# Kernel tuning notes

Hardware: AMD Instinct MI355X
Metric: run time of the kernel (lower is better)

## Reference

```python
import jax, jax.numpy as jnp
import numpy as np

B, C, COUT, L, K = 16, 64, 64, 16384, 3
STRIDE, PAD, DIL, G, DG = 1, 1, 1, 1, 1
LOUT = (L + 2 * PAD - DIL * (K - 1) - 1) // STRIDE + 1


def _conv1d(x, w, b, pad, groups):
    # x: [B, Cin, L], w: [Cout, Cin/groups, k] (torch Conv1d layout)
    y = jax.lax.conv_general_dilated(
        x, w, window_strides=(1,), padding=[(pad, pad)],
        dimension_numbers=('NCH', 'OIH', 'NCH'), feature_group_count=groups)
    return y + b[None, :, None]


def setup_inputs() -> dict:
    key = jax.random.key(0)
    k = jax.random.split(key, 11)
    s = jnp.float32(0.02)  # module init: normal(0, 0.02)
    return {
        'x': jax.random.normal(k[0], (B, C, L), jnp.float32),
        'w_off_dw': jax.random.normal(k[1], (C, 1, 7), jnp.float32) * s,
        'b_off_dw': jax.random.normal(k[2], (C,), jnp.float32) * s,
        'w_off_pw': jax.random.normal(k[3], (G * DG * K, C, 1), jnp.float32) * s,
        'b_off_pw': jax.random.normal(k[4], (G * DG * K,), jnp.float32) * s,
        'w_msk_dw': jax.random.normal(k[5], (C, 1, 7), jnp.float32) * s,
        'b_msk_dw': jax.random.normal(k[6], (C,), jnp.float32) * s,
        'w_msk_pw': jax.random.normal(k[7], (G * DG * K, C, 1), jnp.float32) * s,
        'b_msk_pw': jax.random.normal(k[8], (G * DG * K,), jnp.float32) * s,
        'weight': jax.random.normal(k[9], (COUT, C // G, K), jnp.float32) * s,
        'bias': jax.random.normal(k[10], (COUT,), jnp.float32) * s,
    }


def _deform_conv1d(x, w_off_dw, b_off_dw, w_off_pw, b_off_pw,
                   w_msk_dw, b_msk_dw, w_msk_pw, b_msk_pw, weight, bias):
    # offset / modulation-mask branches: depthwise k=7 conv -> 1x1 conv
    offset = _conv1d(_conv1d(x, w_off_dw, b_off_dw, 3, C), w_off_pw, b_off_pw, 0, 1)  # [B, G*DG*K, Lout]
    mask = jax.nn.sigmoid(_conv1d(_conv1d(x, w_msk_dw, b_msk_dw, 3, C), w_msk_pw, b_msk_pw, 0, 1))

    cpd = C // (G * DG)  # channels per deformable group
    off = jnp.repeat(offset.reshape(B, G * DG, K, LOUT), cpd, axis=1)  # [B, C, K, Lout]
    msk = jnp.repeat(mask.reshape(B, G * DG, K, LOUT), cpd, axis=1)

    base = jnp.arange(LOUT, dtype=x.dtype) * STRIDE - PAD  # [Lout]
    kpos = jnp.arange(K, dtype=x.dtype) * DIL              # [K]
    p = base[None, :] + kpos[:, None]                       # [K, Lout]
    p = p[None, None] + off                                 # fractional sample positions [B, C, K, Lout]

    i0 = jnp.floor(p)
    frac = p - i0
    i0i = i0.astype(jnp.int32)
    i1i = i0i + 1

    xb = jnp.broadcast_to(x[:, :, None, :], (B, C, K, L))
    x0 = jnp.take_along_axis(xb, jnp.clip(i0i, 0, L - 1), axis=-1)
    x1 = jnp.take_along_axis(xb, jnp.clip(i1i, 0, L - 1), axis=-1)
    v0 = ((i0i >= 0) & (i0i < L)).astype(x.dtype)  # zero padding outside
    v1 = ((i1i >= 0) & (i1i < L)).astype(x.dtype)

    # linear interpolation + mask modulation
    val = ((1.0 - frac) * x0 * v0 + frac * x1 * v1) * msk  # [B, C, K, Lout]

    # grouped contraction over (in-channels-per-group, kernel taps)
    out = jnp.einsum('bgikl,goik->bgol',
                     val.reshape(B, G, C // G, K, LOUT),
                     weight.reshape(G, COUT // G, C // G, K))
    return out.reshape(B, COUT, LOUT) + bias[None, :, None]


def reference(x, w_off_dw, b_off_dw, w_off_pw, b_off_pw,
              w_msk_dw, b_msk_dw, w_msk_pw, b_msk_pw, weight, bias):
    return _deform_conv1d(x, w_off_dw, b_off_dw, w_off_pw, b_off_pw,
                          w_msk_dw, b_msk_dw, w_msk_pw, b_msk_pw, weight, bias)
```

## Files before the change

### kernel.cpp

```cpp
#include <hip/hip_runtime.h>
#include <cstdint>

#define LX 16384
#define NB 16
#define LT 64
#define TPB 4
#define HALO 8
#define XI (LT + 2*HALO)
#define XPD 36

typedef __attribute__((ext_vector_type(2))) _Float16 h2;
typedef __attribute__((ext_vector_type(8))) _Float16 h8;
typedef __attribute__((ext_vector_type(4))) unsigned u4;
typedef __attribute__((ext_vector_type(4))) float f4;

static __device__ __forceinline__ h2 u2h(unsigned u) {
    union { unsigned u; h2 h; } v; v.u = u; return v.h;
}
static __device__ __forceinline__ unsigned h2u(h2 h) {
    union { h2 h; unsigned u; } v; v.h = h; return v.u;
}
static __device__ __forceinline__ unsigned pkrtz(float a, float b) {
    auto r = __builtin_amdgcn_cvt_pkrtz(a, b);
    union { decltype(r) h; unsigned u; } v; v.h = r;
    return v.u;
}

#define BAR_LGKM() do { asm volatile("s_waitcnt lgkmcnt(0)" ::: "memory"); \
                        __builtin_amdgcn_s_barrier();                      \
                        asm volatile("" ::: "memory"); } while (0)
#define BAR_RAW()  do { asm volatile("" ::: "memory");                     \
                        __builtin_amdgcn_s_barrier();                      \
                        asm volatile("" ::: "memory"); } while (0)

__global__ void prep_kernel(const float* __restrict__ weight,
                            const float* __restrict__ b_off_pw, const float* __restrict__ w_off_pw,
                            const float* __restrict__ b_off_dw,
                            const float* __restrict__ b_msk_pw, const float* __restrict__ w_msk_pw,
                            const float* __restrict__ b_msk_dw,
                            const float* __restrict__ w_off_dw, const float* __restrict__ w_msk_dw,
                            short* __restrict__ A2, float* __restrict__ beff,
                            unsigned* __restrict__ dwt2, unsigned* __restrict__ pwt2) {
    int bid = blockIdx.x;
    int t = threadIdx.x;
    if (bid < 48) {
        int idx = bid * 256 + t;
        int o = idx / 192;
        int rem = idx - o * 192;
        int tap = rem >> 6, c = rem & 63;
        union { _Float16 h; short s; } v;
        v.h = (_Float16)weight[o * 192 + c * 3 + tap];
        A2[idx] = v.s;
    } else {
        for (int idx = t; idx < 448; idx += 256) {
            int br = idx / 224, r2 = idx - br * 224;
            int j = r2 >> 5, cp = r2 & 31;
            const float* src = br ? w_msk_dw : w_off_dw;
            h2 h; h[0] = (_Float16)src[(2 * cp) * 7 + j]; h[1] = (_Float16)src[(2 * cp + 1) * 7 + j];
            dwt2[idx] = h2u(h);
        }
        if (t < 192) {
            int br = t / 96, r2 = t - br * 96;
            int m = r2 >> 5, cp = r2 & 31;
            const float* src = br ? w_msk_pw : w_off_pw;
            h2 h; h[0] = (_Float16)src[m * 64 + 2 * cp]; h[1] = (_Float16)src[m * 64 + 2 * cp + 1];
            pwt2[t] = h2u(h);
        }
        if (t < 6) {
            int br = t / 3, m = t % 3;
            const float* pw = br ? w_msk_pw : w_off_pw;
            const float* bd = br ? b_msk_dw : b_off_dw;
            const float* bp = br ? b_msk_pw : b_off_pw;
            float s = bp[m];
            for (int c = 0; c < 64; ++c) s += pw[m * 64 + c] * bd[c];
            beff[t] = s;
        }
    }
}

__launch_bounds__(256, 4)
__global__ void deform_main(const float* __restrict__ x,
                            const float* __restrict__ bias,
                            const short* __restrict__ A2,
                            const float* __restrict__ beff,
                            const unsigned* __restrict__ dwt2_g,
                            const unsigned* __restrict__ pwt2_g,
                            float* __restrict__ out) {
    __shared__ __align__(16) unsigned xdw[XI * XPD];
    __shared__ __align__(16) unsigned A2l[6144];
    __shared__ __align__(16) unsigned dwt2[448];
    __shared__ __align__(16) unsigned pwt2[192];
    __shared__ unsigned kl_wp[3][64];
    __shared__ int      kl_li[3][64];
    __shared__ float bias_l[64];
    __shared__ float beff_l[8];

    const int t = threadIdx.x;
    const int lbase = blockIdx.x * (LT * TPB);
    const int b = blockIdx.y;
    const float* xb = x + (size_t)b * (64 * LX);

    f4 rx0[3], rx1[3];

    auto issue_x = [&](int l0v) {
        #pragma unroll
        for (int s = 0; s < 3; ++s) {
            int p = t + 256 * s;
            rx0[s] = (f4){0.f, 0.f, 0.f, 0.f};
            rx1[s] = (f4){0.f, 0.f, 0.f, 0.f};
            if (p < 640) {
                int cp = p & 31, up = p >> 5;
                int g4 = l0v - HALO + up * 4;
                if ((unsigned)g4 < (unsigned)LX) {
                    rx0[s] = *(const f4*)(xb + (size_t)(2 * cp) * LX + g4);
                    rx1[s] = *(const f4*)(xb + (size_t)(2 * cp + 1) * LX + g4);
                }
            }
        }
    };
    auto write_x = [&]() {
        #pragma unroll
        for (int s = 0; s < 3; ++s) {
            int p = t + 256 * s;
            if (p < 640) {
                int cp = p & 31, up = p >> 5;
                #pragma unroll
                for (int d = 0; d < 4; ++d) {
                    int i = up * 4 + d;
                    int pc = ((cp >> 3) + i) & 3;
                    xdw[i * XPD + pc * 8 + (cp & 7)] = pkrtz(rx0[s][d], rx1[s][d]);
                }
            }
        }
    };

    issue_x(lbase);
    {
        const u4* A2g4 = (const u4*)A2;
        #pragma unroll
        for (int s = 0; s < 6; ++s) {
            int idx = t + 256 * s;
            int row = idx / 24;
            int g = idx - row * 24;
            int pdw = row * 96 + ((g * 4) ^ ((row & 7) << 2));
            *(u4*)&A2l[pdw] = A2g4[idx];
        }
    }
    for (int idx = t; idx < 448; idx += 256) dwt2[idx] = dwt2_g[idx];
    if (t < 192) pwt2[t] = pwt2_g[t];
    if (t < 64) bias_l[t] = bias[t];
    if (t < 6)  beff_l[t] = beff[t];
    write_x();
    issue_x(lbase + LT);
    BAR_LGKM();

    #pragma unroll
    for (int tt = 0; tt < TPB; ++tt) {
        const int l0 = lbase + tt * LT;

        {
            const int l = t >> 2, cc = t & 3;
            h2 so2[8], sm2[8];
            #pragma unroll
            for (int m = 0; m < 8; ++m) { so2[m] = (h2)(_Float16)0; sm2[m] = (h2)(_Float16)0; }
            #pragma unroll
            for (int j = 0; j < 7; ++j) {
                int i = l + 5 + j;
                const unsigned* xr = &xdw[i * XPD + (((cc + i) & 3) << 3)];
                u4 xa = *(const u4*)xr;
                u4 xb2 = *(const u4*)(xr + 4);
                const unsigned* wo = &dwt2[j * 32 + cc * 8];
                const unsigned* wm = &dwt2[224 + j * 32 + cc * 8];
                u4 woa = *(const u4*)wo, wob = *(const u4*)(wo + 4);
                u4 wma = *(const u4*)wm, wmb = *(const u4*)(wm + 4);
                #pragma unroll
                for (int m = 0; m < 4; ++m) {
                    so2[m]     += u2h(xa[m])  * u2h(woa[m]);
                    so2[m + 4] += u2h(xb2[m]) * u2h(wob[m]);
                    sm2[m]     += u2h(xa[m])  * u2h(wma[m]);
                    sm2[m + 4] += u2h(xb2[m]) * u2h(wmb[m]);
                }
            }
            float po[3] = {0.f, 0.f, 0.f}, pm[3] = {0.f, 0.f, 0.f};
            #pragma unroll
            for (int m3 = 0; m3 < 3; ++m3) {
                const unsigned* p0 = &pwt2[m3 * 32 + cc * 8];
                const unsigned* p1 = &pwt2[96 + m3 * 32 + cc * 8];
                u4 a0 = *(const u4*)p0, a1 = *(const u4*)(p0 + 4);
                u4 b0 = *(const u4*)p1, b1 = *(const u4*)(p1 + 4);
                #pragma unroll
                for (int m = 0; m < 4; ++m) {
                    po[m3] = __builtin_amdgcn_fdot2(so2[m],     u2h(a0[m]), po[m3], false);
                    po[m3] = __builtin_amdgcn_fdot2(so2[m + 4], u2h(a1[m]), po[m3], false);
                    pm[m3] = __builtin_amdgcn_fdot2(sm2[m],     u2h(b0[m]), pm[m3], false);
                    pm[m3] = __builtin_amdgcn_fdot2(sm2[m + 4], u2h(b1[m]), pm[m3], false);
                }
            }
            #pragma unroll
            for (int d = 1; d <= 2; d <<= 1) {
                #pragma unroll
                for (int m3 = 0; m3 < 3; ++m3) {
                    po[m3] += __shfl_xor(po[m3], d);
                    pm[m3] += __shfl_xor(pm[m3], d);
                }
            }
            if (cc < 3) {
                int k = cc;
                float off = (k == 0 ? po[0] : k == 1 ? po[1] : po[2]) + beff_l[k];
                float z   = (k == 0 ? pm[0] : k == 1 ? pm[1] : pm[2]) + beff_l[3 + k];
                float msk = 1.0f / (1.0f + __expf(-z));
                float p = (float)(l0 + l - 1 + k) + off;
                float fl = floorf(p);
                int i0 = (int)fl, i1 = i0 + 1;
                float fr = p - fl;
                int li0 = i0 - l0 + HALO, li1 = li0 + 1;
                float w0 = (((unsigned)i0 < (unsigned)LX) && ((unsigned)li0 < (unsigned)XI)) ? (1.0f - fr) * msk : 0.0f;
                float w1 = (((unsigned)i1 < (unsigned)LX) && ((unsigned)li1 < (unsigned)XI)) ? fr * msk : 0.0f;
                li0 = min(max(li0, 0), XI - 2);
                kl_wp[k][l] = pkrtz(w0, w1);
                kl_li[k][l] = li0;
            }
        }
        BAR_LGKM();

        {
            const int lane = t & 63;
            const int wv = t >> 6;
            const int r = lane & 15, q = lane >> 4;
            const int lcol = wv * 16 + r;

            h8 bfr[6];
            #pragma unroll
            for (int kk = 0; kk < 6; ++kk) {
                const int tap = kk >> 1;
                unsigned wp = kl_wp[tap][lcol];
                unsigned w00 = __builtin_amdgcn_perm(wp, wp, 0x01000100u);
                unsigned w11 = __builtin_amdgcn_perm(wp, wp, 0x03020302u);
                int li0 = kl_li[tap][lcol];
                int cp0 = (((kk & 1) << 5) + (q << 3)) >> 1;
                int chunkL = cp0 >> 3;
                int o0 = li0 * XPD + ((((chunkL + li0) & 3) << 3) | (cp0 & 7));
                int o1 = (li0 + 1) * XPD + ((((chunkL + li0 + 1) & 3) << 3) | (cp0 & 7));
                u4 r0 = *(const u4*)&xdw[o0];
                u4 r1 = *(const u4*)&xdw[o1];
                u4 xs;
                #pragma unroll
                for (int d = 0; d < 4; ++d)
                    xs[d] = h2u(u2h(r0[d]) * u2h(w00) + u2h(r1[d]) * u2h(w11));
                union { u4 u; h8 h; } cvt; cvt.u = xs;
                bfr[kk] = cvt.h;
            }

            #pragma unroll
            for (int mt = 0; mt < 4; ++mt) {
                f4 acc = {0.f, 0.f, 0.f, 0.f};
                const int row = mt * 16 + r;
                const int rowbase = row * 96;
                const int sw = (r & 7) << 2;
                #pragma unroll
                for (int kk = 0; kk < 6; ++kk) {
                    union { u4 u; h8 h; } af;
                    af.u = *(const u4*)&A2l[rowbase + ((kk * 16 + q * 4) ^ sw)];
                    acc = __builtin_amdgcn_mfma_f32_16x16x32_f16(af.h, bfr[kk], acc, 0, 0, 0);
                }
                int ob = mt * 16 + 4 * q;
                float* op = out + ((size_t)b * 64 + ob) * LX + l0 + lcol;
                #pragma unroll
                for (int e = 0; e < 4; ++e)
                    op[(size_t)e * LX] = acc[e] + bias_l[ob + e];
            }
        }

        if (tt < TPB - 1) {
            BAR_RAW();
            write_x();
            if (tt + 2 < TPB) issue_x(lbase + (tt + 2) * LT);
            BAR_LGKM();
        }
    }
}

extern "C" void kernel_launch(void* const* d_in, const int* in_sizes, int n_in,
                              void* d_out, int out_size, void* d_ws, size_t ws_size,
                              hipStream_t stream) {
    const float* x        = (const float*)d_in[0];
    const float* w_off_dw = (const float*)d_in[1];
    const float* b_off_dw = (const float*)d_in[2];
    const float* w_off_pw = (const float*)d_in[3];
    const float* b_off_pw = (const float*)d_in[4];
    const float* w_msk_dw = (const float*)d_in[5];
    const float* b_msk_dw = (const float*)d_in[6];
    const float* w_msk_pw = (const float*)d_in[7];
    const float* b_msk_pw = (const float*)d_in[8];
    const float* weight   = (const float*)d_in[9];
    const float* bias     = (const float*)d_in[10];
    float* out = (float*)d_out;

    short*    A2   = (short*)d_ws;
    float*    beff = (float*)((char*)d_ws + 24576);
    unsigned* dwt2 = (unsigned*)((char*)d_ws + 24608);
    unsigned* pwt2 = (unsigned*)((char*)d_ws + 26400);

    hipLaunchKernelGGL(prep_kernel, dim3(49), dim3(256), 0, stream,
                       weight, b_off_pw, w_off_pw, b_off_dw, b_msk_pw, w_msk_pw, b_msk_dw,
                       w_off_dw, w_msk_dw, A2, beff, dwt2, pwt2);
    hipLaunchKernelGGL(deform_main, dim3(LX / (LT * TPB), NB), dim3(256), 0, stream,
                       x, bias, A2, beff, dwt2, pwt2, out);
}
```

Before: 154.4 us.

## Fold depthwise+pointwise offset/mask convs into one MFMA and drop LDS staging

Precomputes combined depthwise×pointwise weights so the offset and mask branches become a single 16x16x32 MFMA chain over 7 taps and 64 channels, held as register fragments, replacing the packed-half FMA and fdot2 path. The per-position sample weights and indices are passed between lanes with shuffles instead of through shared memory, which removes a barrier per tile. The main contraction loop is reordered so each interpolated B fragment feeds four accumulators directly. This raises register pressure (14 u4 weight fragments plus 4 accumulators) under the 4-waves launch bound, and the folded weights are rounded to fp16 as products rather than separately.

Measured after the change: 191.2 us. +23.8%, slower.

```diff
diff --git a/kernel.cpp b/kernel.cpp
--- a/kernel.cpp
+++ b/kernel.cpp
@@ -40,7 +40,7 @@
                             const float* __restrict__ b_msk_dw,
                             const float* __restrict__ w_off_dw, const float* __restrict__ w_msk_dw,
                             short* __restrict__ A2, float* __restrict__ beff,
-                            unsigned* __restrict__ dwt2, unsigned* __restrict__ pwt2) {
+                            unsigned* __restrict__ wcg) {
     int bid = blockIdx.x;
     int t = threadIdx.x;
     if (bid < 48) {
@@ -52,27 +52,29 @@
         v.h = (_Float16)weight[o * 192 + c * 3 + tap];
         A2[idx] = v.s;
     } else {
-        for (int idx = t; idx < 448; idx += 256) {
-            int br = idx / 224, r2 = idx - br * 224;
-            int j = r2 >> 5, cp = r2 & 31;
-            const float* src = br ? w_msk_dw : w_off_dw;
-            h2 h; h[0] = (_Float16)src[(2 * cp) * 7 + j]; h[1] = (_Float16)src[(2 * cp + 1) * 7 + j];
-            dwt2[idx] = h2u(h);
-        }
-        if (t < 192) {
-            int br = t / 96, r2 = t - br * 96;
-            int m = r2 >> 5, cp = r2 & 31;
-            const float* src = br ? w_msk_pw : w_off_pw;
-            h2 h; h[0] = (_Float16)src[m * 64 + 2 * cp]; h[1] = (_Float16)src[m * 64 + 2 * cp + 1];
-            pwt2[t] = h2u(h);
+        int lane = t >> 2, d = t & 3;
+        int m = lane & 15, qq = lane >> 4;
+        #pragma unroll
+        for (int s = 0; s < 14; ++s) {
+            int j = s >> 1;
+            int c = (s & 1) * 32 + qq * 8 + 2 * d;
+            float w0 = 0.f, w1 = 0.f;
+            if (m < 3) {
+                w0 = w_off_pw[m * 64 + c]     * w_off_dw[c * 7 + j];
+                w1 = w_off_pw[m * 64 + c + 1] * w_off_dw[(c + 1) * 7 + j];
+            } else if (m < 6) {
+                w0 = w_msk_pw[(m - 3) * 64 + c]     * w_msk_dw[c * 7 + j];
+                w1 = w_msk_pw[(m - 3) * 64 + c + 1] * w_msk_dw[(c + 1) * 7 + j];
+            }
+            wcg[s * 256 + t] = pkrtz(w0, w1);
         }
         if (t < 6) {
-            int br = t / 3, m = t % 3;
+            int br = t / 3, m3 = t % 3;
             const float* pw = br ? w_msk_pw : w_off_pw;
             const float* bd = br ? b_msk_dw : b_off_dw;
             const float* bp = br ? b_msk_pw : b_off_pw;
-            float s = bp[m];
-            for (int c = 0; c < 64; ++c) s += pw[m * 64 + c] * bd[c];
+            float s = bp[m3];
+            for (int c = 0; c < 64; ++c) s += pw[m3 * 64 + c] * bd[c];
             beff[t] = s;
         }
     }
@@ -83,19 +85,17 @@
                             const float* __restrict__ bias,
                             const short* __restrict__ A2,
                             const float* __restrict__ beff,
-                            const unsigned* __restrict__ dwt2_g,
-                            const unsigned* __restrict__ pwt2_g,
+                            const unsigned* __restrict__ wcg,
                             float* __restrict__ out) {
     __shared__ __align__(16) unsigned xdw[XI * XPD];
     __shared__ __align__(16) unsigned A2l[6144];
-    __shared__ __align__(16) unsigned dwt2[448];
-    __shared__ __align__(16) unsigned pwt2[192];
-    __shared__ unsigned kl_wp[3][64];
-    __shared__ int      kl_li[3][64];
     __shared__ float bias_l[64];
     __shared__ float beff_l[8];
 
     const int t = threadIdx.x;
+    const int lane = t & 63;
+    const int wv = t >> 6;
+    const int r = lane & 15, q = lane >> 4;
     const int lbase = blockIdx.x * (LT * TPB);
     const int b = blockIdx.y;
     const float* xb = x + (size_t)b * (64 * LX);
@@ -146,8 +146,12 @@
             *(u4*)&A2l[pdw] = A2g4[idx];
         }
     }
-    for (int idx = t; idx < 448; idx += 256) dwt2[idx] = dwt2_g[idx];
-    if (t < 192) pwt2[t] = pwt2_g[t];
+    u4 wfr[14];
+    {
+        const u4* wc4 = (const u4*)wcg;
+        #pragma unroll
+        for (int s = 0; s < 14; ++s) wfr[s] = wc4[s * 64 + lane];
+    }
     if (t < 64) bias_l[t] = bias[t];
     if (t < 6)  beff_l[t] = beff[t];
     write_x();
@@ -158,56 +162,30 @@
     for (int tt = 0; tt < TPB; ++tt) {
         const int l0 = lbase + tt * LT;
 
+        unsigned mywp = 0; int myli = 0;
         {
-            const int l = t >> 2, cc = t & 3;
-            h2 so2[8], sm2[8];
-            #pragma unroll
-            for (int m = 0; m < 8; ++m) { so2[m] = (h2)(_Float16)0; sm2[m] = (h2)(_Float16)0; }
-            #pragma unroll
-            for (int j = 0; j < 7; ++j) {
-                int i = l + 5 + j;
-                const unsigned* xr = &xdw[i * XPD + (((cc + i) & 3) << 3)];
-                u4 xa = *(const u4*)xr;
-                u4 xb2 = *(const u4*)(xr + 4);
-                const unsigned* wo = &dwt2[j * 32 + cc * 8];
-                const unsigned* wm = &dwt2[224 + j * 32 + cc * 8];
-                u4 woa = *(const u4*)wo, wob = *(const u4*)(wo + 4);
-                u4 wma = *(const u4*)wm, wmb = *(const u4*)(wm + 4);
-                #pragma unroll
-                for (int m = 0; m < 4; ++m) {
-                    so2[m]     += u2h(xa[m])  * u2h(woa[m]);
-                    so2[m + 4] += u2h(xb2[m]) * u2h(wob[m]);
-                    sm2[m]     += u2h(xa[m])  * u2h(wma[m]);
-                    sm2[m + 4] += u2h(xb2[m]) * u2h(wmb[m]);
-                }
-            }
-            float po[3] = {0.f, 0.f, 0.f}, pm[3] = {0.f, 0.f, 0.f};
-            #pragma unroll
-            for (int m3 = 0; m3 < 3; ++m3) {
-                const unsigned* p0 = &pwt2[m3 * 32 + cc * 8];
-                const unsigned* p1 = &pwt2[96 + m3 * 32 + cc * 8];
-                u4 a0 = *(const u4*)p0, a1 = *(const u4*)(p0 + 4);
-                u4 b0 = *(const u4*)p1, b1 = *(const u4*)(p1 + 4);
-                #pragma unroll
-                for (int m = 0; m < 4; ++m) {
-                    po[m3] = __builtin_amdgcn_fdot2(so2[m],     u2h(a0[m]), po[m3], false);
-                    po[m3] = __builtin_amdgcn_fdot2(so2[m + 4], u2h(a1[m]), po[m3], false);
-                    pm[m3] = __builtin_amdgcn_fdot2(sm2[m],     u2h(b0[m]), pm[m3], false);
-                    pm[m3] = __builtin_amdgcn_fdot2(sm2[m + 4], u2h(b1[m]), pm[m3], false);
-                }
-            }
-            #pragma unroll
-            for (int d = 1; d <= 2; d <<= 1) {
-                #pragma unroll
-                for (int m3 = 0; m3 < 3; ++m3) {
-                    po[m3] += __shfl_xor(po[m3], d);
-                    pm[m3] += __shfl_xor(pm[m3], d);
-                }
-            }
-            if (cc < 3) {
-                int k = cc;
-                float off = (k == 0 ? po[0] : k == 1 ? po[1] : po[2]) + beff_l[k];
-                float z   = (k == 0 ? pm[0] : k == 1 ? pm[1] : pm[2]) + beff_l[3 + k];
+            f4 acc2 = {0.f, 0.f, 0.f, 0.f};
+            const int irow = wv * 16 + r + 5;
+            #pragma unroll
+            for (int s = 0; s < 14; ++s) {
+                const int j = s >> 1, half = s & 1;
+                const int i = irow + j;
+                const int chunk = half * 2 + (q >> 1);
+                const int pd = i * XPD + (((chunk + i) & 3) << 3) + ((q & 1) << 2);
+                union { u4 u; h8 h; } bx; bx.u = *(const u4*)&xdw[pd];
+                union { u4 u; h8 h; } ax; ax.u = wfr[s];
+                acc2 = __builtin_amdgcn_mfma_f32_16x16x32_f16(ax.h, bx.h, acc2, 0, 0, 0);
+            }
+            float b0 = __shfl(acc2[0], r);
+            float b1 = __shfl(acc2[1], r);
+            float b2 = __shfl(acc2[2], r);
+            float m0 = __shfl(acc2[3], r);
+            float m1 = __shfl(acc2[0], 16 + r);
+            float m2 = __shfl(acc2[1], 16 + r);
+            if (q < 3) {
+                const int k = q, l = wv * 16 + r;
+                float off = (k == 0 ? b0 : k == 1 ? b1 : b2) + beff_l[k];
+                float z   = (k == 0 ? m0 : k == 1 ? m1 : m2) + beff_l[3 + k];
                 float msk = 1.0f / (1.0f + __expf(-z));
                 float p = (float)(l0 + l - 1 + k) + off;
                 float fl = floorf(p);
@@ -217,27 +195,31 @@
                 float w0 = (((unsigned)i0 < (unsigned)LX) && ((unsigned)li0 < (unsigned)XI)) ? (1.0f - fr) * msk : 0.0f;
                 float w1 = (((unsigned)i1 < (unsigned)LX) && ((unsigned)li1 < (unsigned)XI)) ? fr * msk : 0.0f;
                 li0 = min(max(li0, 0), XI - 2);
-                kl_wp[k][l] = pkrtz(w0, w1);
-                kl_li[k][l] = li0;
-            }
-        }
-        BAR_LGKM();
+                mywp = pkrtz(w0, w1);
+                myli = li0;
+            }
+        }
 
         {
-            const int lane = t & 63;
-            const int wv = t >> 6;
-            const int r = lane & 15, q = lane >> 4;
             const int lcol = wv * 16 + r;
-
-            h8 bfr[6];
+            unsigned wpt[3]; int lit[3];
+            #pragma unroll
+            for (int tap = 0; tap < 3; ++tap) {
+                wpt[tap] = __shfl(mywp, tap * 16 + r);
+                lit[tap] = __shfl(myli, tap * 16 + r);
+            }
+            f4 acc[4];
+            #pragma unroll
+            for (int mt = 0; mt < 4; ++mt) acc[mt] = (f4){0.f, 0.f, 0.f, 0.f};
+            const int sw = (r & 7) << 2;
             #pragma unroll
             for (int kk = 0; kk < 6; ++kk) {
                 const int tap = kk >> 1;
-                unsigned wp = kl_wp[tap][lcol];
+                unsigned wp = wpt[tap];
                 unsigned w00 = __builtin_amdgcn_perm(wp, wp, 0x01000100u);
                 unsigned w11 = __builtin_amdgcn_perm(wp, wp, 0x03020302u);
-                int li0 = kl_li[tap][lcol];
-                int cp0 = (((kk & 1) << 5) + (q << 3)) >> 1;
+                int li0 = lit[tap];
+                int cp0 = ((kk & 1) << 4) + (q << 2);
                 int chunkL = cp0 >> 3;
                 int o0 = li0 * XPD + ((((chunkL + li0) & 3) << 3) | (cp0 & 7));
                 int o1 = (li0 + 1) * XPD + ((((chunkL + li0 + 1) & 3) << 3) | (cp0 & 7));
@@ -247,27 +229,21 @@
                 #pragma unroll
                 for (int d = 0; d < 4; ++d)
                     xs[d] = h2u(u2h(r0[d]) * u2h(w00) + u2h(r1[d]) * u2h(w11));
-                union { u4 u; h8 h; } cvt; cvt.u = xs;
-                bfr[kk] = cvt.h;
-            }
-
+                union { u4 u; h8 h; } bfr; bfr.u = xs;
+                #pragma unroll
+                for (int mt = 0; mt < 4; ++mt) {
+                    union { u4 u; h8 h; } af;
+                    af.u = *(const u4*)&A2l[(mt * 16 + r) * 96 + ((kk * 16 + q * 4) ^ sw)];
+                    acc[mt] = __builtin_amdgcn_mfma_f32_16x16x32_f16(af.h, bfr.h, acc[mt], 0, 0, 0);
+                }
+            }
             #pragma unroll
             for (int mt = 0; mt < 4; ++mt) {
-                f4 acc = {0.f, 0.f, 0.f, 0.f};
-                const int row = mt * 16 + r;
-                const int rowbase = row * 96;
-                const int sw = (r & 7) << 2;
-                #pragma unroll
-                for (int kk = 0; kk < 6; ++kk) {
-                    union { u4 u; h8 h; } af;
-                    af.u = *(const u4*)&A2l[rowbase + ((kk * 16 + q * 4) ^ sw)];
-                    acc = __builtin_amdgcn_mfma_f32_16x16x32_f16(af.h, bfr[kk], acc, 0, 0, 0);
-                }
                 int ob = mt * 16 + 4 * q;
                 float* op = out + ((size_t)b * 64 + ob) * LX + l0 + lcol;
                 #pragma unroll
                 for (int e = 0; e < 4; ++e)
-                    op[(size_t)e * LX] = acc[e] + bias_l[ob + e];
+                    op[(size_t)e * LX] = acc[mt][e] + bias_l[ob + e];
             }
         }
 
@@ -298,12 +274,11 @@
 
     short*    A2   = (short*)d_ws;
     float*    beff = (float*)((char*)d_ws + 24576);
-    unsigned* dwt2 = (unsigned*)((char*)d_ws + 24608);
-    unsigned* pwt2 = (unsigned*)((char*)d_ws + 26400);
+    unsigned* wcg  = (unsigned*)((char*)d_ws + 24608);
 
     hipLaunchKernelGGL(prep_kernel, dim3(49), dim3(256), 0, stream,
                        weight, b_off_pw, w_off_pw, b_off_dw, b_msk_pw, w_msk_pw, b_msk_dw,
-                       w_off_dw, w_msk_dw, A2, beff, dwt2, pwt2);
+                       w_off_dw, w_msk_dw, A2, beff, wcg);
     hipLaunchKernelGGL(deform_main, dim3(LX / (LT * TPB), NB), dim3(256), 0, stream,
-                       x, bias, A2, beff, dwt2, pwt2, out);
-}
+                       x, bias, A2, beff, wcg, out);
+}
```
